# Optimization experiments

Measured on AMD Instinct MI355X. Metric: run time of the kernel, lower is better.

## Reference

```python
import jax, jax.numpy as jnp
import numpy as np

N_NODES = 50000
IN_DIM = 256
OUT_DIM = 128
NUM_HEADS = 2
N_EDGES = 800000


def setup_inputs() -> dict:
    key = jax.random.key(0)
    k1, k2, k3, k4, k5 = jax.random.split(key, 5)
    x = jax.random.normal(k1, (N_NODES, IN_DIM), dtype=jnp.float32)
    edge_index = jax.random.randint(k2, (2, N_EDGES), 0, N_NODES, dtype=jnp.int64)
    # Linear(in_dim, out_dim*num_heads): store weight as [in_dim, out_dim*num_heads]
    fan = IN_DIM + OUT_DIM * NUM_HEADS
    W_w = jax.random.uniform(k3, (IN_DIM, OUT_DIM * NUM_HEADS), dtype=jnp.float32,
                             minval=-np.sqrt(6.0 / fan), maxval=np.sqrt(6.0 / fan))
    W_b = jnp.zeros((OUT_DIM * NUM_HEADS,), dtype=jnp.float32)
    # attention vector a: [2*out_dim], xavier uniform over (1, 2*out_dim)
    fa = 1 + 2 * OUT_DIM
    a = jax.random.uniform(k4, (2 * OUT_DIM,), dtype=jnp.float32,
                           minval=-np.sqrt(6.0 / fa), maxval=np.sqrt(6.0 / fa))
    return {"x": x, "edge_index": edge_index, "W_w": W_w, "W_b": W_b, "a": a}


def _gat_forward(x, edge_index, W_w, W_b, a):
    N = x.shape[0]
    H, D = NUM_HEADS, OUT_DIM
    Wh = (x @ W_w + W_b).reshape(N, H, D)  # [N, H, D]
    src, dst = edge_index[0], edge_index[1]
    a_src, a_dst = a[:D], a[D:]
    # per-node partial scores, then gather -> avoids [E, 2D] concat
    s = jnp.einsum('nhd,d->nh', Wh, a_src)  # [N, H]
    t = jnp.einsum('nhd,d->nh', Wh, a_dst)  # [N, H]
    e = jax.nn.leaky_relu(s[src] + t[dst], negative_slope=0.2)  # [E, H]
    # segment softmax over edges grouped by src node
    m = jax.ops.segment_max(e, src, num_segments=N)  # [N, H], -inf for empty
    ex = jnp.exp(e - m[src])
    denom = jax.ops.segment_sum(ex, src, num_segments=N)  # [N, H]
    alpha = ex / denom[src]  # [E, H]
    # weighted aggregation of destination features into source nodes
    agg = jax.ops.segment_sum(alpha[:, :, None] * Wh[dst], src, num_segments=N)  # [N, H, D]
    deg = jax.ops.segment_sum(jnp.ones_like(src, dtype=Wh.dtype), src, num_segments=N)  # [N]
    h_prime = jnp.where(deg[:, None, None] > 0, agg, Wh)
    return h_prime.reshape(N, H * D)


def reference(x, edge_index, W_w, W_b, a):
    return _gat_forward(x, edge_index, W_w, W_b, a)
```

## Files before the change

### kernel.cpp

```cpp
#include <hip/hip_runtime.h>
#include <hip/hip_bf16.h>
#include <math.h>

#define N_NODES 50000
#define IN_DIM 256
#define OUT_DIM 128
#define NUM_HEADS 2
#define N_EDGES 800000
#define F (OUT_DIM*NUM_HEADS)
#define SCAN_B 1024
#define N_SB ((N_NODES + SCAN_B - 1) / SCAN_B)
#define LDSP 264
#define CAP 128

typedef __bf16 bf16;
typedef __bf16 bf16x8 __attribute__((ext_vector_type(8)));
typedef float  f32x4  __attribute__((ext_vector_type(4)));

__global__ void k_transpose(const float* __restrict__ W, bf16* __restrict__ Wt,
                            int* __restrict__ deg) {
    int k = blockIdx.x;
    int n = threadIdx.x;
    Wt[(size_t)n*IN_DIM + k] = (bf16)W[(size_t)k*F + n];
    int id = blockIdx.x * F + threadIdx.x;
    if (id < N_NODES) deg[id] = 0;
}

__global__ __launch_bounds__(256) void k_gemm(const float* __restrict__ X,
                                              const bf16* __restrict__ Wt,
                                              const float* __restrict__ Wb,
                                              const float* __restrict__ Av,
                                              bf16* __restrict__ Wh,
                                              float* __restrict__ s_arr,
                                              float* __restrict__ t_arr) {
    __shared__ bf16 As[64 * LDSP];
    __shared__ float sS[2][64], sT[2][64];
    int t = threadIdx.x;
    int wave = t >> 6, lane = t & 63;
    int quad = lane >> 4, l16 = lane & 15;
    int row0 = blockIdx.x * 64;
    int col0 = wave * 64;
    int h = wave >> 1;

    {
        int rr = t >> 5;
        int cc = (t & 31) * 8;
        #pragma unroll
        for (int i = 0; i < 8; ++i) {
            int r = row0 + 8*i + rr;
            r = (r < N_NODES) ? r : (N_NODES - 1);
            const float* p = X + (size_t)r * IN_DIM + cc;
            f32x4 lo = *(const f32x4*)p;
            f32x4 hi = *(const f32x4*)(p + 4);
            bf16x8 pk;
            #pragma unroll
            for (int q = 0; q < 4; ++q) {
                pk[q]   = (bf16)lo[q];
                pk[q+4] = (bf16)hi[q];
            }
            *(bf16x8*)(As + (8*i + rr) * LDSP + cc) = pk;
        }
    }
    if (t < 128) { sS[t >> 6][t & 63] = 0.f; sT[t >> 6][t & 63] = 0.f; }
    __syncthreads();

    f32x4 acc[4][4] = {};
    #pragma unroll
    for (int ks = 0; ks < 8; ++ks) {
        int kb = ks * 32;
        bf16x8 bfrag[4];
        #pragma unroll
        for (int ni = 0; ni < 4; ++ni)
            bfrag[ni] = *(const bf16x8*)(Wt + (size_t)(col0 + ni*16 + l16)*IN_DIM
                                            + kb + quad*8);
        bf16x8 afrag[4];
        #pragma unroll
        for (int mi = 0; mi < 4; ++mi)
            afrag[mi] = *(const bf16x8*)(As + (mi*16 + l16)*LDSP + kb + quad*8);

        #pragma unroll
        for (int mi = 0; mi < 4; ++mi)
            #pragma unroll
            for (int ni = 0; ni < 4; ++ni)
                acc[mi][ni] = __builtin_amdgcn_mfma_f32_16x16x32_bf16(
                                  afrag[mi], bfrag[ni], acc[mi][ni], 0, 0, 0);
    }

    float bias_l[4], as_l[4], at_l[4];
    #pragma unroll
    for (int ni = 0; ni < 4; ++ni) {
        int c = col0 + ni*16 + l16;
        int d = c & (OUT_DIM - 1);
        bias_l[ni] = Wb[c];
        as_l[ni]   = Av[d];
        at_l[ni]   = Av[OUT_DIM + d];
    }

    #pragma unroll
    for (int mi = 0; mi < 4; ++mi) {
        #pragma unroll
        for (int reg = 0; reg < 4; ++reg) {
            int rl  = mi*16 + quad*4 + reg;
            int row = row0 + rl;
            float ps = 0.f, pt = 0.f;
            #pragma unroll
            for (int ni = 0; ni < 4; ++ni) {
                float val = acc[mi][ni][reg] + bias_l[ni];
                if (row < N_NODES)
                    Wh[(size_t)row*F + col0 + ni*16 + l16] = (bf16)val;
                ps += val * as_l[ni];
                pt += val * at_l[ni];
            }
            #pragma unroll
            for (int m = 8; m >= 1; m >>= 1) {
                ps += __shfl_xor(ps, m);
                pt += __shfl_xor(pt, m);
            }
            if ((lane & 15) == 0) {
                atomicAdd(&sS[h][rl], ps);
                atomicAdd(&sT[h][rl], pt);
            }
        }
    }
    __syncthreads();
    if (t < 128) {
        int hh = t >> 6, rl = t & 63;
        int n = row0 + rl;
        if (n < N_NODES) {
            s_arr[n*2 + hh] = sS[hh][rl];
            t_arr[n*2 + hh] = sT[hh][rl];
        }
    }
}

__global__ void k_hist(const int* __restrict__ src, int* __restrict__ deg) {
    int e = blockIdx.x * 256 + threadIdx.x;
    if (e < N_EDGES) atomicAdd(&deg[src[e]], 1);
}

__global__ __launch_bounds__(SCAN_B) void k_scan_local(const int* __restrict__ deg,
                                                       int* __restrict__ incl,
                                                       int* __restrict__ bsum) {
    __shared__ int lds[SCAN_B];
    int t = threadIdx.x;
    int i = blockIdx.x * SCAN_B + t;
    int v = (i < N_NODES) ? deg[i] : 0;
    lds[t] = v;
    __syncthreads();
    for (int off = 1; off < SCAN_B; off <<= 1) {
        int u = (t >= off) ? lds[t - off] : 0;
        __syncthreads();
        lds[t] += u;
        __syncthreads();
    }
    if (i < N_NODES) incl[i] = lds[t];
    if (t == SCAN_B - 1) bsum[blockIdx.x] = lds[t];
}

__global__ __launch_bounds__(256) void k_scan_final(const int* __restrict__ incl,
                                                    const int* __restrict__ deg,
                                                    const int* __restrict__ bsum,
                                                    int* __restrict__ row_start,
                                                    int* __restrict__ cursor) {
    __shared__ int sboff[64];
    int t = threadIdx.x;
    if (t < 64) {
        int orig = (t < N_SB) ? bsum[t] : 0;
        int v = orig;
        #pragma unroll
        for (int off = 1; off < 64; off <<= 1) {
            int u = __shfl_up(v, off);
            if (t >= off) v += u;
        }
        sboff[t] = v - orig;
        if (t == 63 && blockIdx.x == 0) row_start[N_NODES] = v;
    }
    __syncthreads();
    int i = blockIdx.x * 256 + t;
    if (i < N_NODES) {
        int excl = incl[i] - deg[i] + sboff[i >> 10];
        row_start[i] = excl;
        cursor[i]    = excl;
    }
}

__global__ void k_scatter(const int* __restrict__ src, const int* __restrict__ dst,
                          int* __restrict__ cursor, int* __restrict__ sorted_dst) {
    int e = blockIdx.x * 256 + threadIdx.x;
    if (e < N_EDGES) {
        int s = src[e];
        int pos = atomicAdd(&cursor[s], 1);
        sorted_dst[pos] = dst[e];
    }
}

__global__ __launch_bounds__(256) void k_agg(const bf16* __restrict__ Wh,
                                             const float* __restrict__ s_arr,
                                             const float* __restrict__ t_arr,
                                             const int* __restrict__ row_start,
                                             const int* __restrict__ sdst,
                                             float* __restrict__ out) {
    __shared__ float sp0[4][CAP];
    __shared__ float sp1[4][CAP];
    __shared__ int   sd[4][CAP];
    int wave = threadIdx.x >> 6, lane = threadIdx.x & 63;
    int n = blockIdx.x * 4 + wave;
    int sub = lane >> 5, cl = lane & 31;
    int c = cl * 8, h = cl >> 4;
    int beg = row_start[n], end = row_start[n + 1];
    if (beg == end) {
        if (sub == 0) {
            bf16x8 wh = *(const bf16x8*)(Wh + (size_t)n*F + c);
            f32x4 o0, o1;
            #pragma unroll
            for (int i = 0; i < 4; ++i) { o0[i] = (float)wh[i]; o1[i] = (float)wh[4+i]; }
            *(f32x4*)(out + (size_t)n*F + c)     = o0;
            *(f32x4*)(out + (size_t)n*F + c + 4) = o1;
        }
        return;
    }
    float2 sv = ((const float2*)s_arr)[n];
    float sum0 = 0.f, sum1 = 0.f;
    float a[8] = {0,0,0,0,0,0,0,0};
    float bacc[8] = {0,0,0,0,0,0,0,0};
    const float* sph = h ? sp1[wave] : sp0[wave];

    for (int c0 = beg; c0 < end; c0 += CAP) {
        int cnt = min(CAP, end - c0);
        for (int j = lane; j < cnt; j += 64) {
            int d = sdst[c0 + j];
            float2 tv = ((const float2*)t_arr)[d];
            float e0 = sv.x + tv.x; e0 = (e0 >= 0.f) ? e0 : 0.2f * e0;
            float e1 = sv.y + tv.y; e1 = (e1 >= 0.f) ? e1 : 0.2f * e1;
            float p0 = __expf(e0), p1 = __expf(e1);
            sp0[wave][j] = p0;
            sp1[wave][j] = p1;
            sd[wave][j]  = d;
            sum0 += p0;
            sum1 += p1;
        }
        int j = 0;
        for (; j + 8 <= cnt; j += 8) {
            int j0 = j + sub, j1 = j + 2 + sub, j2 = j + 4 + sub, j3 = j + 6 + sub;
            int d0 = sd[wave][j0], d1 = sd[wave][j1];
            int d2 = sd[wave][j2], d3 = sd[wave][j3];
            float p0 = sph[j0], p1 = sph[j1], p2 = sph[j2], p3 = sph[j3];
            bf16x8 w0 = *(const bf16x8*)(Wh + (size_t)d0*F + c);
            bf16x8 w1 = *(const bf16x8*)(Wh + (size_t)d1*F + c);
            bf16x8 w2 = *(const bf16x8*)(Wh + (size_t)d2*F + c);
            bf16x8 w3 = *(const bf16x8*)(Wh + (size_t)d3*F + c);
            #pragma unroll
            for (int i = 0; i < 8; ++i) {
                a[i]    += p0 * (float)w0[i];
                bacc[i] += p1 * (float)w1[i];
                a[i]    += p2 * (float)w2[i];
                bacc[i] += p3 * (float)w3[i];
            }
        }
        for (; j < cnt; j += 2) {
            int jj = j + sub;
            int jc = (jj < cnt) ? jj : 0;
            float p = (jj < cnt) ? sph[jc] : 0.f;
            int d = sd[wave][jc];
            bf16x8 w = *(const bf16x8*)(Wh + (size_t)d*F + c);
            #pragma unroll
            for (int i = 0; i < 8; ++i) a[i] += p * (float)w[i];
        }
    }
    #pragma unroll
    for (int m = 32; m >= 1; m >>= 1) {
        sum0 += __shfl_xor(sum0, m);
        sum1 += __shfl_xor(sum1, m);
    }
    float inv = 1.f / (h ? sum1 : sum0);
    #pragma unroll
    for (int i = 0; i < 8; ++i) {
        a[i] += bacc[i];
        a[i] += __shfl_xor(a[i], 32);
    }
    if (sub == 0) {
        f32x4 o0, o1;
        #pragma unroll
        for (int i = 0; i < 4; ++i) { o0[i] = a[i] * inv; o1[i] = a[4+i] * inv; }
        *(f32x4*)(out + (size_t)n*F + c)     = o0;
        *(f32x4*)(out + (size_t)n*F + c + 4) = o1;
    }
}

extern "C" void kernel_launch(void* const* d_in, const int* in_sizes, int n_in,
                              void* d_out, int out_size, void* d_ws, size_t ws_size,
                              hipStream_t stream) {
    const float* x  = (const float*)d_in[0];
    const int*   ei = (const int*)d_in[1];
    const float* Ww = (const float*)d_in[2];
    const float* Wb = (const float*)d_in[3];
    const float* a  = (const float*)d_in[4];
    float* out = (float*)d_out;
    const int* src = ei;
    const int* dst = ei + N_EDGES;

    char* ws = (char*)d_ws;
    bf16*  Wh        = (bf16*)ws;   ws += (size_t)N_NODES * F * 2;
    bf16*  Wt        = (bf16*)ws;   ws += (size_t)IN_DIM * F * 2;
    float* s_arr     = (float*)ws;  ws += (size_t)N_NODES * 2 * 4;
    float* t_arr     = (float*)ws;  ws += (size_t)N_NODES * 2 * 4;
    int*   deg       = (int*)ws;    ws += (size_t)N_NODES * 4;
    int*   incl      = (int*)ws;    ws += (size_t)N_NODES * 4;
    int*   bsum      = (int*)ws;    ws += 64 * 4;
    int*   row_start = (int*)ws;    ws += (size_t)(N_NODES + 1) * 4 + 12;
    int*   cursor    = (int*)ws;    ws += (size_t)N_NODES * 4;
    int*   sdst      = (int*)ws;    ws += (size_t)N_EDGES * 4;

    k_transpose<<<IN_DIM, F, 0, stream>>>(Ww, Wt, deg);
    k_gemm<<<(N_NODES + 63) / 64, 256, 0, stream>>>(x, Wt, Wb, a, Wh, s_arr, t_arr);
    k_hist<<<(N_EDGES + 255) / 256, 256, 0, stream>>>(src, deg);
    k_scan_local<<<N_SB, SCAN_B, 0, stream>>>(deg, incl, bsum);
    k_scan_final<<<(N_NODES + 255) / 256, 256, 0, stream>>>(incl, deg, bsum, row_start, cursor);
    k_scatter<<<(N_EDGES + 255) / 256, 256, 0, stream>>>(src, dst, cursor, sdst);
    k_agg<<<N_NODES / 4, 256, 0, stream>>>(Wh, s_arr, t_arr, row_start, sdst, out);
}
```

Before: 275.5 us.

## Fuse degree histogram into GEMM and stage Wh stores through LDS

The separate degree-histogram kernel is removed and its edge loop runs as a grid-stride loop at the start of the GEMM kernel, saving one launch and letting the atomics overlap with GEMM work. The GEMM epilogue now writes the bf16 Wh tile into the reused LDS buffer and then stores it to global memory as coalesced 16-byte row vectors, replacing scattered 2-byte stores. This adds two barriers, LDS traffic and extra latency in each GEMM block from the atomic loop.

```diff
diff --git a/kernel.cpp b/kernel.cpp
--- a/kernel.cpp
+++ b/kernel.cpp
@@ -30,6 +30,8 @@
                                               const bf16* __restrict__ Wt,
                                               const float* __restrict__ Wb,
                                               const float* __restrict__ Av,
+                                              const int* __restrict__ src,
+                                              int* __restrict__ deg,
                                               bf16* __restrict__ Wh,
                                               float* __restrict__ s_arr,
                                               float* __restrict__ t_arr) {
@@ -43,6 +45,13 @@
     int h = wave >> 1;
 
     {
+        int gid = blockIdx.x * 256 + t;
+        int gsz = gridDim.x * 256;
+        for (int e = gid; e < N_EDGES; e += gsz)
+            atomicAdd(&deg[src[e]], 1);
+    }
+
+    {
         int rr = t >> 5;
         int cc = (t & 31) * 8;
         #pragma unroll
@@ -100,14 +109,11 @@
     for (int mi = 0; mi < 4; ++mi) {
         #pragma unroll
         for (int reg = 0; reg < 4; ++reg) {
-            int rl  = mi*16 + quad*4 + reg;
-            int row = row0 + rl;
+            int rl = mi*16 + quad*4 + reg;
             float ps = 0.f, pt = 0.f;
             #pragma unroll
             for (int ni = 0; ni < 4; ++ni) {
                 float val = acc[mi][ni][reg] + bias_l[ni];
-                if (row < N_NODES)
-                    Wh[(size_t)row*F + col0 + ni*16 + l16] = (bf16)val;
                 ps += val * as_l[ni];
                 pt += val * at_l[ni];
             }
@@ -122,7 +128,32 @@
             }
         }
     }
-    __syncthreads();
+
+    __syncthreads();
+    #pragma unroll
+    for (int mi = 0; mi < 4; ++mi)
+        #pragma unroll
+        for (int ni = 0; ni < 4; ++ni) {
+            int cc = col0 + ni*16 + l16;
+            #pragma unroll
+            for (int reg = 0; reg < 4; ++reg) {
+                int rl = mi*16 + quad*4 + reg;
+                As[rl*LDSP + cc] = (bf16)(acc[mi][ni][reg] + bias_l[ni]);
+            }
+        }
+    __syncthreads();
+
+    #pragma unroll
+    for (int i = 0; i < 8; ++i) {
+        int idx = i * 2048 + t * 8;
+        int row = idx >> 8;
+        int cc  = idx & 255;
+        bf16x8 v = *(const bf16x8*)(As + row*LDSP + cc);
+        int grow = row0 + row;
+        if (grow < N_NODES)
+            *(bf16x8*)(Wh + (size_t)grow*F + cc) = v;
+    }
+
     if (t < 128) {
         int hh = t >> 6, rl = t & 63;
         int n = row0 + rl;
@@ -131,11 +162,6 @@
             t_arr[n*2 + hh] = sT[hh][rl];
         }
     }
-}
-
-__global__ void k_hist(const int* __restrict__ src, int* __restrict__ deg) {
-    int e = blockIdx.x * 256 + threadIdx.x;
-    if (e < N_EDGES) atomicAdd(&deg[src[e]], 1);
 }
 
 __global__ __launch_bounds__(SCAN_B) void k_scan_local(const int* __restrict__ deg,
@@ -312,8 +338,8 @@
     int*   sdst      = (int*)ws;    ws += (size_t)N_EDGES * 4;
 
     k_transpose<<<IN_DIM, F, 0, stream>>>(Ww, Wt, deg);
-    k_gemm<<<(N_NODES + 63) / 64, 256, 0, stream>>>(x, Wt, Wb, a, Wh, s_arr, t_arr);
-    k_hist<<<(N_EDGES + 255) / 256, 256, 0, stream>>>(src, deg);
+    k_gemm<<<(N_NODES + 63) / 64, 256, 0, stream>>>(x, Wt, Wb, a, src, deg,
+                                                    Wh, s_arr, t_arr);
     k_scan_local<<<N_SB, SCAN_B, 0, stream>>>(deg, incl, bsum);
     k_scan_final<<<(N_NODES + 255) / 256, 256, 0, stream>>>(incl, deg, bsum, row_start, cursor);
     k_scatter<<<(N_EDGES + 255) / 256, 256, 0, stream>>>(src, dst, cursor, sdst);
```

Result: no change. 272.9 us (-1.0%).
